# Kernel optimization log

Hardware: AMD Instinct MI355X
Metric: run time of the kernel (lower is better)

Reference implementation:

```python
import math
import jax, jax.numpy as jnp
import numpy as np

B, T, C, H, DQK, DV = 2, 2048, 1024, 16, 64, 64


def setup_inputs() -> dict:
    key = jax.random.key(0)
    ks = jax.random.split(key, 5)
    x = jax.random.normal(ks[0], (B, T, C), dtype=jnp.float32)
    # randw: randn(*d) / sqrt(d[-1])
    w_q = jax.random.normal(ks[1], (H, DQK, C), dtype=jnp.float32) / math.sqrt(C)
    w_k = jax.random.normal(ks[2], (H, DQK, C), dtype=jnp.float32) / math.sqrt(C)
    w_v = jax.random.normal(ks[3], (H, DV, C), dtype=jnp.float32) / math.sqrt(C)
    w_o = jax.random.normal(ks[4], (DV * H, C), dtype=jnp.float32) / math.sqrt(C)
    return {"x": x, "w_q": w_q, "w_k": w_k, "w_v": w_v, "w_o": w_o}


def reference(x, w_q, w_k, w_v, w_o):
    # Full-sequence causal forward (bs_q.first == 0, nb == T): caches are
    # fully written in one shot, so they reduce to the plain projections.
    n, t, c = x.shape
    q = jnp.einsum('ntc,hdc->nhtd', x, w_q)
    k = jnp.einsum('ntc,hdc->nhtd', x, w_k)
    v = jnp.einsum('ntc,hdc->nhtd', x, w_v)
    scale = 1.0 / math.sqrt(w_q.shape[1])
    a = jnp.einsum('nhtd,nhsd->nhts', q, k) * scale  # [n,h,t,s]
    causal = jnp.arange(t)[:, None] < jnp.arange(t)[None, :]  # True above diag
    a = jnp.where(causal[None, None, :, :], -jnp.inf, a)
    a = jax.nn.softmax(a, axis=3)
    y = jnp.einsum('nhts,nhsd->nthd', a, v).reshape(n, t, -1)  # [n,t,h*dv]
    return y @ w_o  # cache_y, [n,t,c]
```

## Files before the change

kernel.cpp:

```cpp
#include <hip/hip_runtime.h>


typedef short bf16x4 __attribute__((ext_vector_type(4)));
typedef short bf16x8 __attribute__((ext_vector_type(8)));
typedef float f32x4 __attribute__((ext_vector_type(4)));

#define MFMA_BF16 __builtin_amdgcn_mfma_f32_16x16x32_bf16

#define QSCALE 0.18033688011112042f

__device__ __forceinline__ unsigned short f2bf(float f) {
    union { float f; unsigned u; } un; un.f = f;
    unsigned r = un.u + 0x7fffu + ((un.u >> 16) & 1u);
    return (unsigned short)(r >> 16);
}
__device__ __forceinline__ unsigned pk2(float a, float b) {
    return (unsigned)f2bf(a) | ((unsigned)f2bf(b) << 16);
}
__device__ __forceinline__ unsigned pk2t(float a, float b) {
    union { float f; unsigned u; } ua, ub; ua.f = a; ub.f = b;
    return (ua.u >> 16) | (ub.u & 0xffff0000u);
}
__device__ __forceinline__ void gload16(const void* g, void* l) {
    __builtin_amdgcn_global_load_lds(
        (const __attribute__((address_space(1))) unsigned int*)g,
        (__attribute__((address_space(3))) unsigned int*)l, 16, 0, 0);
}

__global__ __launch_bounds__(256) void prep(
    const float* __restrict__ x, const float* __restrict__ wq,
    const float* __restrict__ wk, const float* __restrict__ wv,
    const float* __restrict__ wo,
    unsigned short* __restrict__ x16, unsigned short* __restrict__ wq16,
    unsigned short* __restrict__ wk16, unsigned short* __restrict__ wv16,
    unsigned short* __restrict__ wot)
{
    const int bid = blockIdx.x;
    if (bid < 3584) {
        const float* s; unsigned short* d; int off;
        if (bid < 2048)      { s = x;  d = x16;  off = bid * 2048; }
        else if (bid < 2560) { s = wq; d = wq16; off = (bid - 2048) * 2048; }
        else if (bid < 3072) { s = wk; d = wk16; off = (bid - 2560) * 2048; }
        else                 { s = wv; d = wv16; off = (bid - 3072) * 2048; }
        int i = off + threadIdx.x * 8;
        float4 f0 = *(const float4*)&s[i], f1 = *(const float4*)&s[i + 4];
        uint4 o;
        o.x = pk2(f0.x, f0.y); o.y = pk2(f0.z, f0.w);
        o.z = pk2(f1.x, f1.y); o.w = pk2(f1.z, f1.w);
        *(uint4*)&d[i] = o;
    } else {
        __shared__ unsigned short t[64 * 72];
        const int b2 = bid - 3584;
        const int k0 = (b2 & 15) << 6, n0 = (b2 >> 4) << 6;
        const int r = threadIdx.x >> 2, cg = (threadIdx.x & 3) << 4;
        const float* src = &wo[(k0 + r) * 1024 + n0 + cg];
        #pragma unroll
        for (int j = 0; j < 16; j += 4) {
            float4 f = *(const float4*)&src[j];
            t[(cg + j + 0) * 72 + r] = f2bf(f.x);
            t[(cg + j + 1) * 72 + r] = f2bf(f.y);
            t[(cg + j + 2) * 72 + r] = f2bf(f.z);
            t[(cg + j + 3) * 72 + r] = f2bf(f.w);
        }
        __syncthreads();
        unsigned short* dst = &wot[(n0 + r) * 1024 + k0 + cg];
        unsigned short* tr = &t[r * 72 + cg];
        unsigned v[16];
        #pragma unroll
        for (int j = 0; j < 16; ++j) v[j] = tr[j];
        uint4 o0, o1;
        o0.x = v[0] | (v[1] << 16);   o0.y = v[2] | (v[3] << 16);
        o0.z = v[4] | (v[5] << 16);   o0.w = v[6] | (v[7] << 16);
        o1.x = v[8] | (v[9] << 16);   o1.y = v[10] | (v[11] << 16);
        o1.z = v[12] | (v[13] << 16); o1.w = v[14] | (v[15] << 16);
        *(uint4*)&dst[0] = o0;
        *(uint4*)&dst[8] = o1;
    }
}

__device__ __forceinline__ void gemm_body(
    const unsigned short* __restrict__ A, const unsigned short* __restrict__ Bm,
    void* __restrict__ C, int m0, int n0, int mode, int ldc, float sc)
{
    __shared__ unsigned short sa[2][128 * 32];
    __shared__ unsigned short sb[2][128 * 32];
    const int tid = threadIdx.x, wave = tid >> 6, lane = tid & 63;
    const int l15 = lane & 15, l4 = lane >> 4;
    const int wm = (wave >> 1) << 6, wn = (wave & 1) << 6;

    const int r16 = lane >> 2;
    const int gcol = (((lane & 3) ^ ((r16 >> 1) & 3)) << 3);
    const int rcol = (l4 ^ ((l15 >> 1) & 3)) << 3;
    const unsigned short* Ag0 = &A[(size_t)(m0 + wave * 16 + r16) * 1024 + gcol];
    const unsigned short* Ag1 = Ag0 + (size_t)64 * 1024;
    const unsigned short* Bg0 = &Bm[(size_t)(n0 + wave * 16 + r16) * 1024 + gcol];
    const unsigned short* Bg1 = Bg0 + (size_t)64 * 1024;
    const int lb0 = (wave * 16) * 32;
    const int lb1 = (64 + wave * 16) * 32;

    gload16(Ag0, &sa[0][lb0]);
    gload16(Ag1, &sa[0][lb1]);
    gload16(Bg0, &sb[0][lb0]);
    gload16(Bg1, &sb[0][lb1]);
    __syncthreads();

    f32x4 acc[4][4] = {};

    #pragma unroll
    for (int kk = 0; kk < 32; ++kk) {
        const int cur = kk & 1;
        if (kk < 31) {
            const int off = (kk + 1) * 32;
            const int nxt = 1 - cur;
            gload16(Ag0 + off, &sa[nxt][lb0]);
            gload16(Ag1 + off, &sa[nxt][lb1]);
            gload16(Bg0 + off, &sb[nxt][lb0]);
            gload16(Bg1 + off, &sb[nxt][lb1]);
        }
        bf16x8 af[4], bf4[4];
        #pragma unroll
        for (int i = 0; i < 4; ++i)
            af[i] = *(const bf16x8*)&sa[cur][(wm + i * 16 + l15) * 32 + rcol];
        #pragma unroll
        for (int j = 0; j < 4; ++j)
            bf4[j] = *(const bf16x8*)&sb[cur][(wn + j * 16 + l15) * 32 + rcol];
        #pragma unroll
        for (int i = 0; i < 4; ++i)
            #pragma unroll
            for (int j = 0; j < 4; ++j)
                acc[i][j] = MFMA_BF16(af[i], bf4[j], acc[i][j], 0, 0, 0);
        __syncthreads();
    }

    #pragma unroll
    for (int i = 0; i < 4; ++i)
        #pragma unroll
        for (int j = 0; j < 4; ++j)
            #pragma unroll
            for (int r = 0; r < 4; ++r) {
                int row = m0 + wm + i * 16 + l4 * 4 + r;
                int col = n0 + wn + j * 16 + l15;
                float val = acc[i][j][r];
                if (mode == 0) {
                    int nb = row >> 11, t = row & 2047;
                    int hh = col >> 6, dd = col & 63;
                    ((unsigned short*)C)[(((nb << 4) + hh) * 2048 + t) * 64 + dd] =
                        f2bf(val * sc);
                } else if (mode == 1) {
                    ((float*)C)[(size_t)row * ldc + col] = val;
                } else {
                    int s = col & 31;
                    int cp = (col & ~31) | (((s >> 2) & 3) << 3)
                                         | (((s >> 4) & 1) << 2) | (s & 3);
                    ((unsigned short*)C)[(size_t)row * ldc + cp] = f2bf(val);
                }
            }
}

__global__ __launch_bounds__(256) void proj(
    const unsigned short* __restrict__ x16,
    const unsigned short* __restrict__ wq16,
    const unsigned short* __restrict__ wk16,
    const unsigned short* __restrict__ wv16,
    unsigned short* __restrict__ qbuf,
    unsigned short* __restrict__ kbuf,
    unsigned short* __restrict__ vtb)
{
    const int bid = blockIdx.x;
    if (bid < 512) {
        int m0 = (bid & 31) << 7;
        int n0g = (bid >> 5) << 7;
        if (n0g < 1024)
            gemm_body(x16, wq16, qbuf, m0, n0g, 0, 0, QSCALE);
        else
            gemm_body(x16, wk16, kbuf, m0, n0g - 1024, 0, 0, 1.0f);
    } else {
        int v = bid - 512;
        gemm_body(wv16, x16, vtb, (v & 7) << 7, (v >> 3) << 7, 2, 4096, 1.0f);
    }
}

__global__ __launch_bounds__(256) void outp(
    const unsigned short* __restrict__ ybuf,
    const unsigned short* __restrict__ wot,
    float* __restrict__ out)
{
    __shared__ unsigned short sa[2][64 * 32];
    __shared__ unsigned short sb[2][64 * 32];
    const int tid = threadIdx.x, wave = tid >> 6, lane = tid & 63;
    const int l15 = lane & 15, l4 = lane >> 4;
    const int bid = blockIdx.x;
    const int m0 = (bid & 63) << 6, n0 = (bid >> 6) << 6;

    const int r16 = lane >> 2;
    const int gcol = (((lane & 3) ^ ((r16 >> 1) & 3)) << 3);
    const int rcol = (l4 ^ ((l15 >> 1) & 3)) << 3;
    const unsigned short* Ag = &ybuf[(size_t)(m0 + wave * 16 + r16) * 1024 + gcol];
    const unsigned short* Bg = &wot[(size_t)(n0 + wave * 16 + r16) * 1024 + gcol];
    const int lb = (wave * 16) * 32;

    gload16(Ag, &sa[0][lb]);
    gload16(Bg, &sb[0][lb]);
    __syncthreads();

    f32x4 acc[4] = {};

    #pragma unroll
    for (int kk = 0; kk < 32; ++kk) {
        const int cur = kk & 1;
        if (kk < 31) {
            const int off = (kk + 1) * 32;
            gload16(Ag + off, &sa[1 - cur][lb]);
            gload16(Bg + off, &sb[1 - cur][lb]);
        }
        bf16x8 af = *(const bf16x8*)&sa[cur][(wave * 16 + l15) * 32 + rcol];
        #pragma unroll
        for (int j = 0; j < 4; ++j) {
            bf16x8 bf = *(const bf16x8*)&sb[cur][(j * 16 + l15) * 32 + rcol];
            acc[j] = MFMA_BF16(af, bf, acc[j], 0, 0, 0);
        }
        __syncthreads();
    }

    #pragma unroll
    for (int j = 0; j < 4; ++j)
        #pragma unroll
        for (int r = 0; r < 4; ++r) {
            int row = m0 + wave * 16 + l4 * 4 + r;
            int col = n0 + j * 16 + l15;
            out[(size_t)row * 1024 + col] = acc[j][r];
        }
}

__global__ __launch_bounds__(256) void attn(
    const unsigned short* __restrict__ q,
    const unsigned short* __restrict__ k,
    const unsigned short* __restrict__ vt,
    unsigned short* __restrict__ y)
{
    constexpr int P = 72;
    __shared__ unsigned short sk[2][64 * P];
    __shared__ unsigned short sv[2][64 * P];
    const int tid = threadIdx.x, wave = tid >> 6, lane = tid & 63;
    const int l15 = lane & 15, l4 = lane >> 4;
    const int bid = blockIdx.x;
    const int qtt = (bid < 512) ? (31 - (bid >> 5)) : ((bid - 512) >> 5);
    const int bh = bid & 31;
    const int nb = bh >> 4, hh = bh & 15;
    const int q0 = qtt << 6;
    const size_t base = (size_t)bh << 17;

    const int r0 = tid >> 3, c0 = (tid & 7) << 3;
    const unsigned short* kg = &k[base + ((size_t)r0 << 6) + c0];
    const unsigned short* vg = &vt[(size_t)((hh << 6) + r0) * 4096 + (nb << 11) + c0];
    const int lk0 = r0 * P + c0, lk1 = (r0 + 32) * P + c0;

    bf16x8 qf[2];
    #pragma unroll
    for (int ks = 0; ks < 2; ++ks)
        qf[ks] = *(const bf16x8*)
            &q[base + (size_t)(q0 + wave * 16 + l15) * 64 + ks * 32 + l4 * 8];

    float l_sum = 0.f;
    f32x4 acc[4] = {};

    const int nst = qtt + 1;

    {
        uint4 ka = *(const uint4*)(kg);
        uint4 kb = *(const uint4*)(kg + (32 << 6));
        uint4 va = *(const uint4*)(vg);
        uint4 vb = *(const uint4*)(vg + 32 * 4096);
        *(uint4*)&sk[0][lk0] = ka;  *(uint4*)&sk[0][lk1] = kb;
        *(uint4*)&sv[0][lk0] = va;  *(uint4*)&sv[0][lk1] = vb;
    }
    __syncthreads();

    auto step = [&](const int cur, const int st, const bool more) {
        uint4 ka, kb, va, vb;
        if (more) {
            const int s1 = (st + 1) << 6;
            ka = *(const uint4*)(kg + ((size_t)s1 << 6));
            kb = *(const uint4*)(kg + ((size_t)(s1 + 32) << 6));
            va = *(const uint4*)(vg + s1);
            vb = *(const uint4*)(vg + 32 * 4096 + s1);
        }

        f32x4 s_acc[4] = {};
        #pragma unroll
        for (int ks = 0; ks < 2; ++ks)
            #pragma unroll
            for (int ns = 0; ns < 4; ++ns) {
                bf16x8 kf = *(const bf16x8*)&sk[cur][(ns * 16 + l15) * P + ks * 32 + l4 * 8];
                s_acc[ns] = MFMA_BF16(kf, qf[ks], s_acc[ns], 0, 0, 0);
            }

        if (st == qtt) {
            const int ql = wave * 16 + l15;
            #pragma unroll
            for (int ns = 0; ns < 4; ++ns) {
                #pragma unroll
                for (int r = 0; r < 4; ++r)
                    if (ns * 16 + l4 * 4 + r > ql) s_acc[ns][r] = -1e30f;
            }
        }

        float pe[4][4];
        #pragma unroll
        for (int ns = 0; ns < 4; ++ns) {
            #pragma unroll
            for (int r = 0; r < 4; ++r) pe[ns][r] = exp2f(s_acc[ns][r]);
            l_sum += (pe[ns][0] + pe[ns][1]) + (pe[ns][2] + pe[ns][3]);
        }

        #pragma unroll
        for (int ks = 0; ks < 2; ++ks) {
            uint4 pw;
            pw.x = pk2t(pe[2 * ks][0], pe[2 * ks][1]);
            pw.y = pk2t(pe[2 * ks][2], pe[2 * ks][3]);
            pw.z = pk2t(pe[2 * ks + 1][0], pe[2 * ks + 1][1]);
            pw.w = pk2t(pe[2 * ks + 1][2], pe[2 * ks + 1][3]);
            bf16x8 pf = *(bf16x8*)&pw;
            #pragma unroll
            for (int ds = 0; ds < 4; ++ds) {
                bf16x8 vf = *(const bf16x8*)
                    &sv[cur][(ds * 16 + l15) * P + ks * 32 + l4 * 8];
                acc[ds] = MFMA_BF16(vf, pf, acc[ds], 0, 0, 0);
            }
        }

        if (more) {
            const int nxt = cur ^ 1;
            *(uint4*)&sk[nxt][lk0] = ka;  *(uint4*)&sk[nxt][lk1] = kb;
            *(uint4*)&sv[nxt][lk0] = va;  *(uint4*)&sv[nxt][lk1] = vb;
        }
        __syncthreads();
    };

    int st = 0;
    for (; st + 2 <= nst; st += 2) {
        step(0, st, true);
        step(1, st + 1, (st + 2) < nst);
    }
    if (st < nst) step(0, st, false);

    l_sum += __shfl_xor(l_sum, 16);
    l_sum += __shfl_xor(l_sum, 32);
    const float rl = __builtin_amdgcn_rcpf(l_sum);

    const size_t rowbase =
        ((size_t)((nb << 11) + q0 + wave * 16 + l15) << 10) + (hh << 6) + l4 * 4;
    #pragma unroll
    for (int ds = 0; ds < 4; ++ds) {
        uint2 o;
        o.x = pk2(acc[ds][0] * rl, acc[ds][1] * rl);
        o.y = pk2(acc[ds][2] * rl, acc[ds][3] * rl);
        *(uint2*)&y[rowbase + ds * 16] = o;
    }
}

extern "C" void kernel_launch(void* const* d_in, const int* in_sizes, int n_in,
                              void* d_out, int out_size, void* d_ws, size_t ws_size,
                              hipStream_t stream) {
    const float* x  = (const float*)d_in[0];
    const float* wq = (const float*)d_in[1];
    const float* wk = (const float*)d_in[2];
    const float* wv = (const float*)d_in[3];
    const float* wo = (const float*)d_in[4];
    float* out = (float*)d_out;

    const size_t M1 = 1u << 20;
    unsigned short* x16  = (unsigned short*)d_ws;
    unsigned short* wq16 = x16 + 4 * M1;
    unsigned short* wk16 = wq16 + M1;
    unsigned short* wv16 = wk16 + M1;
    unsigned short* wot  = wv16 + M1;
    unsigned short* qbuf = wot + M1;
    unsigned short* kbuf = qbuf + 4 * M1;
    unsigned short* vtb  = kbuf + 4 * M1;
    unsigned short* ybuf = vtb + 4 * M1;

    dim3 blk(256);
    prep<<<3840, blk, 0, stream>>>(x, wq, wk, wv, wo, x16, wq16, wk16, wv16, wot);
    proj<<<768, blk, 0, stream>>>(x16, wq16, wk16, wv16, qbuf, kbuf, vtb);
    attn<<<1024, blk, 0, stream>>>(qbuf, kbuf, vtb, ybuf);
    outp<<<1024, blk, 0, stream>>>(ybuf, wot, out);
}
```

Before: 170.9 us.

## Load attention K/V tiles directly to LDS with XOR-swizzled layout

Replaces the register-staged K/V tile copies in the attention kernel with direct global-to-LDS loads (global_load_lds). The padded row stride is swapped for an unpadded 64-wide layout with an XOR chunk swizzle, so the MFMA fragment reads avoid bank conflicts. This frees VGPRs, removes the ds_write instructions, and lets the next tile's prefetch proceed asynchronously during compute. The risk is that the prefetch into the other buffer now has no explicit wait before the end-of-step barrier, so correctness depends on the compiler inserting vmcnt waits.

```diff
diff --git a/kernel.cpp b/kernel.cpp
--- a/kernel.cpp
+++ b/kernel.cpp
@@ -238,9 +238,8 @@
     const unsigned short* __restrict__ vt,
     unsigned short* __restrict__ y)
 {
-    constexpr int P = 72;
-    __shared__ unsigned short sk[2][64 * P];
-    __shared__ unsigned short sv[2][64 * P];
+    __shared__ unsigned short sk[2][64 * 64];
+    __shared__ unsigned short sv[2][64 * 64];
     const int tid = threadIdx.x, wave = tid >> 6, lane = tid & 63;
     const int l15 = lane & 15, l4 = lane >> 4;
     const int bid = blockIdx.x;
@@ -250,10 +249,14 @@
     const int q0 = qtt << 6;
     const size_t base = (size_t)bh << 17;
 
-    const int r0 = tid >> 3, c0 = (tid & 7) << 3;
-    const unsigned short* kg = &k[base + ((size_t)r0 << 6) + c0];
-    const unsigned short* vg = &vt[(size_t)((hh << 6) + r0) * 4096 + (nb << 11) + c0];
-    const int lk0 = r0 * P + c0, lk1 = (r0 + 32) * P + c0;
+    const int lrow = lane >> 3;
+    const int gch = ((lane & 7) ^ lrow) << 3;
+    const int row0 = wave * 8 + lrow, row1 = 32 + wave * 8 + lrow;
+    const unsigned short* kg0 = &k[base + (size_t)row0 * 64 + gch];
+    const unsigned short* kg1 = &k[base + (size_t)row1 * 64 + gch];
+    const unsigned short* vg0 = &vt[(size_t)((hh << 6) + row0) * 4096 + (nb << 11) + gch];
+    const unsigned short* vg1 = &vt[(size_t)((hh << 6) + row1) * 4096 + (nb << 11) + gch];
+    const int lbk0 = (wave * 8) * 64, lbk1 = (32 + wave * 8) * 64;
 
     bf16x8 qf[2];
     #pragma unroll
@@ -266,34 +269,33 @@
 
     const int nst = qtt + 1;
 
-    {
-        uint4 ka = *(const uint4*)(kg);
-        uint4 kb = *(const uint4*)(kg + (32 << 6));
-        uint4 va = *(const uint4*)(vg);
-        uint4 vb = *(const uint4*)(vg + 32 * 4096);
-        *(uint4*)&sk[0][lk0] = ka;  *(uint4*)&sk[0][lk1] = kb;
-        *(uint4*)&sv[0][lk0] = va;  *(uint4*)&sv[0][lk1] = vb;
-    }
+    const int rch0 = ((0 + l4) ^ (l15 & 7)) << 3;
+    const int rch1 = ((4 + l4) ^ (l15 & 7)) << 3;
+
+    gload16(kg0, &sk[0][lbk0]);
+    gload16(kg1, &sk[0][lbk1]);
+    gload16(vg0, &sv[0][lbk0]);
+    gload16(vg1, &sv[0][lbk1]);
     __syncthreads();
 
     auto step = [&](const int cur, const int st, const bool more) {
-        uint4 ka, kb, va, vb;
         if (more) {
-            const int s1 = (st + 1) << 6;
-            ka = *(const uint4*)(kg + ((size_t)s1 << 6));
-            kb = *(const uint4*)(kg + ((size_t)(s1 + 32) << 6));
-            va = *(const uint4*)(vg + s1);
-            vb = *(const uint4*)(vg + 32 * 4096 + s1);
+            const int nxt = cur ^ 1;
+            const int s1e = (st + 1) << 6;
+            gload16(kg0 + ((size_t)s1e << 6), &sk[nxt][lbk0]);
+            gload16(kg1 + ((size_t)s1e << 6), &sk[nxt][lbk1]);
+            gload16(vg0 + s1e, &sv[nxt][lbk0]);
+            gload16(vg1 + s1e, &sv[nxt][lbk1]);
         }
 
         f32x4 s_acc[4] = {};
         #pragma unroll
-        for (int ks = 0; ks < 2; ++ks)
-            #pragma unroll
-            for (int ns = 0; ns < 4; ++ns) {
-                bf16x8 kf = *(const bf16x8*)&sk[cur][(ns * 16 + l15) * P + ks * 32 + l4 * 8];
-                s_acc[ns] = MFMA_BF16(kf, qf[ks], s_acc[ns], 0, 0, 0);
-            }
+        for (int ns = 0; ns < 4; ++ns) {
+            bf16x8 kf0 = *(const bf16x8*)&sk[cur][(ns * 16 + l15) * 64 + rch0];
+            bf16x8 kf1 = *(const bf16x8*)&sk[cur][(ns * 16 + l15) * 64 + rch1];
+            s_acc[ns] = MFMA_BF16(kf0, qf[0], s_acc[ns], 0, 0, 0);
+            s_acc[ns] = MFMA_BF16(kf1, qf[1], s_acc[ns], 0, 0, 0);
+        }
 
         if (st == qtt) {
             const int ql = wave * 16 + l15;
@@ -321,18 +323,12 @@
             pw.z = pk2t(pe[2 * ks + 1][0], pe[2 * ks + 1][1]);
             pw.w = pk2t(pe[2 * ks + 1][2], pe[2 * ks + 1][3]);
             bf16x8 pf = *(bf16x8*)&pw;
+            const int rch = ks ? rch1 : rch0;
             #pragma unroll
             for (int ds = 0; ds < 4; ++ds) {
-                bf16x8 vf = *(const bf16x8*)
-                    &sv[cur][(ds * 16 + l15) * P + ks * 32 + l4 * 8];
+                bf16x8 vf = *(const bf16x8*)&sv[cur][(ds * 16 + l15) * 64 + rch];
                 acc[ds] = MFMA_BF16(vf, pf, acc[ds], 0, 0, 0);
             }
-        }
-
-        if (more) {
-            const int nxt = cur ^ 1;
-            *(uint4*)&sk[nxt][lk0] = ka;  *(uint4*)&sk[nxt][lk1] = kb;
-            *(uint4*)&sv[nxt][lk0] = va;  *(uint4*)&sv[nxt][lk1] = vb;
         }
         __syncthreads();
     };
```

Measured after the change: 170.1 us. About the same (-0.5%).
